# Optimization experiments

Hardware: AMD Instinct MI355X
Metric: run time of the kernel (lower is better)

The kernel has to match this reference:

```python
import jax, jax.numpy as jnp
import numpy as np
import math

B, L, C, H, CP = 2, 512, 576, 8, 128
C3 = C // 3            # 192
DK = C // H            # 72
DK3 = DK // 3          # 24
DIV = math.sqrt(DK)


def _ln(x, w, b, eps=1e-6):
    m = jnp.mean(x, axis=-1, keepdims=True)
    v = jnp.mean(jnp.square(x - m), axis=-1, keepdims=True)
    return (x - m) * jax.lax.rsqrt(v + eps) * w + b


def setup_inputs() -> dict:
    key = jax.random.key(0)
    ks = jax.random.split(key, 12)
    s = 0.05
    def n(k, shape):
        return jax.random.normal(k, shape, jnp.float32) * s
    return {
        "x": jax.random.normal(ks[0], (B, L, C), jnp.float32),
        "pairX": jax.random.normal(ks[1], (B, L, L, CP), jnp.float32),
        "g": jnp.ones((1,), jnp.float32),
        "ln1_w": jnp.ones((C,), jnp.float32), "ln1_b": jnp.zeros((C,), jnp.float32),
        "ln2_w": jnp.ones((CP,), jnp.float32), "ln2_b": jnp.zeros((CP,), jnp.float32),
        "Wq": n(ks[2], (C3, C3)), "bq": jnp.zeros((C3,), jnp.float32),
        "Wk": n(ks[3], (C3, C3)), "bk": jnp.zeros((C3,), jnp.float32),
        "Wv": n(ks[4], (C3, C3)), "bv": jnp.zeros((C3,), jnp.float32),
        "Wg": n(ks[5], (C3, C3)), "bg": jnp.zeros((C3,), jnp.float32),
        "conv_w": n(ks[6], (3, H, H, 5, 5)), "conv_b": jnp.zeros((3, H), jnp.float32),
        "Wp": n(ks[7], (CP, H)), "bp": jnp.zeros((H,), jnp.float32),
        "Wpr": n(ks[8], (H, CP)), "bpr": jnp.zeros((CP,), jnp.float32),
        "Wo": n(ks[9], (C, C)), "bo": jnp.zeros((C,), jnp.float32),
    }


def reference(x, pairX, g, ln1_w, ln1_b, ln2_w, ln2_b, Wq, bq, Wk, bk, Wv, bv,
              Wg, bg, conv_w, conv_b, Wp, bp, Wpr, bpr, Wo, bo):
    ori_x = x
    xn = _ln(x, ln1_w, ln1_b)                      # [B,L,C]
    pn = _ln(pairX, ln2_w, ln2_b)                  # [B,L,L,CP]

    # split channels into 3 groups: [B,3,L,C3]
    xs = xn.reshape(B, L, 3, C3).transpose(0, 2, 1, 3)

    def proj(W, b):
        y = xs @ W + b                              # [B,3,L,C3]
        return y.reshape(B, 3, L, H, DK3).transpose(0, 1, 3, 2, 4)  # [B,3,H,L,DK3]

    q = proj(Wq, bq)
    k = proj(Wk, bk)
    v = proj(Wv, bv)
    gate = proj(Wg, bg)

    qkMatrix = jnp.einsum('bchld,bchmd->bchlm', q, k)  # [B,3,H,L,L]
    pairBias = (pn @ Wp + bp).transpose(0, 3, 1, 2)[:, None]  # [B,1,H,L,L]
    oriQK = qkMatrix + pairBias                     # [B,3,H,L,L]

    # 3-channel 5x5 conv refinement, summed over the 3 branches -> [B,1,H,L,L]
    dn = ('NCHW', 'OIHW', 'NCHW')
    convQK = sum(
        jax.lax.conv_general_dilated(oriQK[:, i], conv_w[i], (1, 1), 'SAME',
                                     dimension_numbers=dn)
        + conv_b[i][None, :, None, None]
        for i in range(3)
    )[:, None]

    qk = (oriQK + convQK) / DIV                     # [B,3,H,L,L]
    score = jax.nn.softmax(qk, axis=-1)
    h_outs = jnp.einsum('bchlm,bchmd->bchld', score, v) * jax.nn.sigmoid(gate)
    h_outs = h_outs.transpose(0, 3, 1, 2, 4).reshape(B, L, C)

    rawScoreMean = jax.nn.gelu(jnp.mean(qk, axis=1).transpose(0, 2, 3, 1),
                               approximate=False)   # [B,L,L,H]
    out1 = (h_outs @ Wo + bo) + ori_x * g
    out2 = rawScoreMean @ Wpr + bpr                 # [B,L,L,CP]
    return out1, out2
```

## Files before the change

kernel.cpp:

```cpp
#include <hip/hip_runtime.h>
#include <hip/hip_bf16.h>

#define BDIM 2
#define LDIM 512
#define CDIM 576
#define HDIM 8
#define CPD  128
#define DK3  24
#define INV_DIV 0.117851130197757920f

static constexpr size_t OFF_Q    = 0;
static constexpr size_t OFF_K    = 589824;
static constexpr size_t OFF_V    = 1179648;
static constexpr size_t OFF_G    = 1769472;
static constexpr size_t OFF_BIAS = 2359296;
static constexpr size_t OFF_ORI  = OFF_BIAS + 4194304;
static constexpr size_t OFF_QK   = OFF_ORI + 12582912;
static constexpr size_t OFF_H    = OFF_QK + 12582912;
static constexpr size_t OFF_WPH  = OFF_H + 589824;
static constexpr size_t OFF_CS   = OFF_WPH + 1024;
static constexpr size_t OFF_XN   = OFF_QK;

__device__ __forceinline__ float gelu_exact(float v) {
    return 0.5f * v * (1.f + erff(v * 0.70710678118654752f));
}

__global__ __launch_bounds__(256) void k_prep(
    const float* __restrict__ ln2w, const float* __restrict__ ln2b,
    const float* __restrict__ Wp, const float* __restrict__ bp,
    float* __restrict__ wph, float* __restrict__ csum)
{
    __shared__ float wl[1024];
    const int tid = threadIdx.x;
    for (int i = tid; i < 1024; i += 256) {
        int h = i >> 7, d = i & 127;
        float v = ln2w[d] * Wp[d * 8 + h];
        wl[i] = v; wph[i] = v;
    }
    __syncthreads();
    const int h = tid >> 5, c4 = tid & 31;
    float p = wl[h * 128 + c4 * 4] + wl[h * 128 + c4 * 4 + 1]
            + wl[h * 128 + c4 * 4 + 2] + wl[h * 128 + c4 * 4 + 3];
#pragma unroll
    for (int o = 1; o < 32; o <<= 1) p += __shfl_xor(p, o);
    if (c4 == 0) csum[h] = p;
    float q = 0.f;
#pragma unroll
    for (int k = 0; k < 4; ++k) { int d = c4 * 4 + k; q = fmaf(ln2b[d], Wp[d * 8 + h], q); }
#pragma unroll
    for (int o = 1; o < 32; o <<= 1) q += __shfl_xor(q, o);
    if (c4 == 0) csum[8 + h] = q + bp[h];
}

__global__ __launch_bounds__(256) void k_ln(
    const float* __restrict__ x, const float* __restrict__ ln1w, const float* __restrict__ ln1b,
    float* __restrict__ xn)
{
    const int tid = threadIdx.x;
    const int wid = tid >> 6, lane = tid & 63;
    const int row = blockIdx.x * 4 + wid;
    const float* xr = x + (size_t)row * CDIM;
    float vals[9]; float s = 0.f, sq = 0.f;
#pragma unroll
    for (int u = 0; u < 9; ++u) {
        float v = xr[lane + 64 * u];
        vals[u] = v; s += v; sq += v * v;
    }
#pragma unroll
    for (int o = 32; o; o >>= 1) { s += __shfl_xor(s, o); sq += __shfl_xor(sq, o); }
    float m = s * (1.f / 576.f);
    float inv = rsqrtf(sq * (1.f / 576.f) - m * m + 1e-6f);
    float* xo = xn + (size_t)row * CDIM;
#pragma unroll
    for (int u = 0; u < 9; ++u) {
        int idx = lane + 64 * u;
        xo[idx] = (vals[u] - m) * inv * ln1w[idx] + ln1b[idx];
    }
}

__global__ __launch_bounds__(256) void k_proj(
    const float* __restrict__ xn,
    const float* __restrict__ Wq, const float* __restrict__ bq,
    const float* __restrict__ Wk, const float* __restrict__ bk,
    const float* __restrict__ Wv, const float* __restrict__ bv,
    const float* __restrict__ Wg, const float* __restrict__ bg,
    float* __restrict__ qo, float* __restrict__ ko, float* __restrict__ vo, float* __restrict__ go)
{
    __shared__ float As[192 * 64];
    __shared__ float Bs[32 * 192];
    const int tid = threadIdx.x;
    const int bx = blockIdx.x;
    const int mi = bx / 48, rem = bx % 48;
    const int g = rem >> 4, rb = rem & 15;
    const int row0 = rb * 64;

    const float* W  = mi == 0 ? Wq : mi == 1 ? Wk : mi == 2 ? Wv : Wg;
    const float* bb = mi == 0 ? bq : mi == 1 ? bk : mi == 2 ? bv : bg;
    float* op       = mi == 0 ? qo : mi == 1 ? ko : mi == 2 ? vo : go;

    {
        const int r = tid & 63, k4b = tid >> 6;
#pragma unroll
        for (int it = 0; it < 12; ++it) {
            int k4 = k4b + it * 4;
            float4 v = *(const float4*)&xn[(size_t)(row0 + r) * 576 + g * 192 + k4 * 4];
            As[(k4 * 4 + 0) * 64 + r] = v.x;
            As[(k4 * 4 + 1) * 64 + r] = v.y;
            As[(k4 * 4 + 2) * 64 + r] = v.z;
            As[(k4 * 4 + 3) * 64 + r] = v.w;
        }
    }

    const int rg = tid >> 4, cg = tid & 15;
    const int r0 = rg * 4, c0 = cg * 12;
    float acc[4][12] = {};

    for (int kk = 0; kk < 192; kk += 32) {
        __syncthreads();
#pragma unroll
        for (int i = 0; i < 6; ++i) {
            int f = tid + 256 * i;
            int k2 = f / 48, c4 = f % 48;
            *(float4*)&Bs[k2 * 192 + c4 * 4] = *(const float4*)&W[(size_t)(kk + k2) * 192 + c4 * 4];
        }
        __syncthreads();
#pragma unroll
        for (int k2 = 0; k2 < 32; ++k2) {
            const float4 a  = *(const float4*)&As[(kk + k2) * 64 + r0];
            const float4 b0 = *(const float4*)&Bs[k2 * 192 + c0];
            const float4 b1 = *(const float4*)&Bs[k2 * 192 + c0 + 4];
            const float4 b2 = *(const float4*)&Bs[k2 * 192 + c0 + 8];
            const float ar[4] = {a.x, a.y, a.z, a.w};
#pragma unroll
            for (int r = 0; r < 4; ++r) {
                acc[r][0] = fmaf(ar[r], b0.x, acc[r][0]);
                acc[r][1] = fmaf(ar[r], b0.y, acc[r][1]);
                acc[r][2] = fmaf(ar[r], b0.z, acc[r][2]);
                acc[r][3] = fmaf(ar[r], b0.w, acc[r][3]);
                acc[r][4] = fmaf(ar[r], b1.x, acc[r][4]);
                acc[r][5] = fmaf(ar[r], b1.y, acc[r][5]);
                acc[r][6] = fmaf(ar[r], b1.z, acc[r][6]);
                acc[r][7] = fmaf(ar[r], b1.w, acc[r][7]);
                acc[r][8] = fmaf(ar[r], b2.x, acc[r][8]);
                acc[r][9] = fmaf(ar[r], b2.y, acc[r][9]);
                acc[r][10] = fmaf(ar[r], b2.z, acc[r][10]);
                acc[r][11] = fmaf(ar[r], b2.w, acc[r][11]);
            }
        }
    }

    const int h = cg >> 1, d24 = (cg & 1) * 12;
    const float4 bj0 = *(const float4*)&bb[c0];
    const float4 bj1 = *(const float4*)&bb[c0 + 4];
    const float4 bj2 = *(const float4*)&bb[c0 + 8];
#pragma unroll
    for (int r = 0; r < 4; ++r) {
        int row = row0 + r0 + r;
        int b = row >> 9, l = row & 511;
        float* o = op + ((((size_t)b * 3 + g) * HDIM + h) * LDIM + l) * DK3 + d24;
        *(float4*)(o + 0) = make_float4(acc[r][0] + bj0.x, acc[r][1] + bj0.y,
                                        acc[r][2] + bj0.z, acc[r][3] + bj0.w);
        *(float4*)(o + 4) = make_float4(acc[r][4] + bj1.x, acc[r][5] + bj1.y,
                                        acc[r][6] + bj1.z, acc[r][7] + bj1.w);
        *(float4*)(o + 8) = make_float4(acc[r][8] + bj2.x, acc[r][9] + bj2.y,
                                        acc[r][10] + bj2.z, acc[r][11] + bj2.w);
    }
}

__global__ __launch_bounds__(256) void k_pairbias(
    const float* __restrict__ pairX, const float* __restrict__ wph,
    const float* __restrict__ csum, float* __restrict__ bias)
{
    const int row = blockIdx.x * 256 + threadIdx.x;
    const float* rp = pairX + (size_t)row * CPD;

    float acc[8] = {};
    float sum = 0.f, sumsq = 0.f;
    for (int s = 0; s < 8; ++s) {
        float rr[16];
        *(float4*)&rr[0]  = *(const float4*)(rp + s * 16 + 0);
        *(float4*)&rr[4]  = *(const float4*)(rp + s * 16 + 4);
        *(float4*)&rr[8]  = *(const float4*)(rp + s * 16 + 8);
        *(float4*)&rr[12] = *(const float4*)(rp + s * 16 + 12);
#pragma unroll
        for (int k = 0; k < 16; ++k) { sum += rr[k]; sumsq = fmaf(rr[k], rr[k], sumsq); }
        const float* wp_s = wph + s * 16;
#pragma unroll
        for (int h = 0; h < 8; ++h) {
            const float* w = wp_s + h * 128;
#pragma unroll
            for (int k = 0; k < 16; ++k) acc[h] = fmaf(rr[k], w[k], acc[h]);
        }
    }
    const float m = sum * (1.f / 128.f);
    const float inv = rsqrtf(sumsq * (1.f / 128.f) - m * m + 1e-6f);
    const int b = row >> 18;
    const int ij = row & 262143;
    float* bo = bias + ((size_t)b << 21) + ij;
#pragma unroll
    for (int h = 0; h < 8; ++h) {
        float o = inv * (acc[h] - m * csum[h]) + csum[8 + h];
        bo[(size_t)h << 18] = o;
    }
}

__global__ __launch_bounds__(256) void k_qkmat(
    const float* __restrict__ q, const float* __restrict__ k,
    const float* __restrict__ bias, float* __restrict__ oriQK)
{
    __shared__ float Kl[512 * 28];
    __shared__ float Ql[32 * 28];
    const int tid = threadIdx.x;
    const int bch = blockIdx.x >> 4;
    const int itile = blockIdx.x & 15;
    const float* kp = k + (size_t)bch * 512 * 24;
    const float* qp = q + (size_t)bch * 512 * 24 + (size_t)itile * 32 * 24;
    for (int idx = tid; idx < 512 * 24; idx += 256) {
        int j = idx / 24, d = idx - j * 24;
        Kl[j * 28 + d] = kp[idx];
    }
    for (int idx = tid; idx < 32 * 24; idx += 256) {
        int i = idx / 24, d = idx - i * 24;
        Ql[i * 28 + d] = qp[idx];
    }
    __syncthreads();

    const int ti = tid >> 4, tj = tid & 15;
    const int b = bch / 24, h = bch & 7;
    const float* biasp = bias + ((size_t)(b * 8 + h) * 512 + itile * 32) * 512;
    float* outp = oriQK + (size_t)bch * 262144 + (size_t)itile * 32 * 512;

    for (int cc = 0; cc < 4; ++cc) {
        float acc[2][8] = {};
#pragma unroll
        for (int d4 = 0; d4 < 6; ++d4) {
            const float4 q0 = *(const float4*)&Ql[(ti * 2 + 0) * 28 + d4 * 4];
            const float4 q1 = *(const float4*)&Ql[(ti * 2 + 1) * 28 + d4 * 4];
#pragma unroll
            for (int u = 0; u < 8; ++u) {
                const float4 kv = *(const float4*)&Kl[(cc * 128 + u * 16 + tj) * 28 + d4 * 4];
                acc[0][u] = fmaf(q0.x, kv.x, fmaf(q0.y, kv.y, fmaf(q0.z, kv.z, fmaf(q0.w, kv.w, acc[0][u]))));
                acc[1][u] = fmaf(q1.x, kv.x, fmaf(q1.y, kv.y, fmaf(q1.z, kv.z, fmaf(q1.w, kv.w, acc[1][u]))));
            }
        }
#pragma unroll
        for (int r = 0; r < 2; ++r) {
            int i = ti * 2 + r;
#pragma unroll
            for (int u = 0; u < 8; ++u) {
                int j = cc * 128 + u * 16 + tj;
                outp[(size_t)i * 512 + j] = acc[r][u] + biasp[(size_t)i * 512 + j];
            }
        }
    }
}

__global__ __launch_bounds__(256, 3) void k_conv(
    const float* __restrict__ oriQK, const float* __restrict__ convW, const float* __restrict__ convB,
    const float* __restrict__ Wpr, const float* __restrict__ bpr,
    float* __restrict__ qk, float* __restrict__ out2)
{
    __shared__ float smem[8 * 36 * 40];
    float* tile = smem;
    const int tid = threadIdx.x;
    const int bx = blockIdx.x;
    const int b = bx >> 8, rem = bx & 255;
    const int i0 = (rem >> 4) * 32, j0 = (rem & 15) * 32;

    const int jg = tid & 7, ii = tid >> 3;
    const int j4 = jg * 4;
    float acc[8][4] = {};
    float cen[3][8][4];

    for (int c = 0; c < 3; ++c) {
        __syncthreads();
        for (int idx = tid; idx < 8 * 1296; idx += 256) {
            int ch = idx / 1296;
            int r = idx - ch * 1296;
            int iw = r / 36, jw = r - iw * 36;
            int gi = i0 - 2 + iw, gj = j0 - 2 + jw;
            float v = 0.f;
            if ((unsigned)gi < 512u && (unsigned)gj < 512u)
                v = oriQK[((size_t)(b * 24 + c * 8 + ch) << 18) + ((size_t)gi << 9) + gj];
            tile[ch * 1440 + iw * 40 + jw] = v;
        }
        __syncthreads();

        const float* wb = convW + c * 1600;
        for (int hi = 0; hi < 8; ++hi) {
            const float* tch = &tile[hi * 1440];
#pragma unroll
            for (int kh = 0; kh < 5; ++kh) {
                const float* trow = &tch[(ii + kh) * 40 + j4];
                float v[8];
                *(float4*)&v[0] = *(const float4*)&trow[0];
                *(float4*)&v[4] = *(const float4*)&trow[4];
                if (kh == 2) {
                    cen[c][hi][0] = v[2]; cen[c][hi][1] = v[3];
                    cen[c][hi][2] = v[4]; cen[c][hi][3] = v[5];
                }
#pragma unroll
                for (int kw = 0; kw < 5; ++kw) {
                    const float* wt = wb + hi * 25 + kh * 5 + kw;
                    const float w0 = wt[0],    w1 = wt[200],  w2 = wt[400],  w3 = wt[600];
                    const float w4 = wt[800],  w5 = wt[1000], w6 = wt[1200], w7 = wt[1400];
#pragma unroll
                    for (int j = 0; j < 4; ++j) {
                        float vv = v[kw + j];
                        acc[0][j] = fmaf(w0, vv, acc[0][j]);
                        acc[1][j] = fmaf(w1, vv, acc[1][j]);
                        acc[2][j] = fmaf(w2, vv, acc[2][j]);
                        acc[3][j] = fmaf(w3, vv, acc[3][j]);
                        acc[4][j] = fmaf(w4, vv, acc[4][j]);
                        acc[5][j] = fmaf(w5, vv, acc[5][j]);
                        acc[6][j] = fmaf(w6, vv, acc[6][j]);
                        acc[7][j] = fmaf(w7, vv, acc[7][j]);
                    }
                }
            }
        }
    }
    __syncthreads();

    float* gql = smem;
    const int gi = i0 + ii, gj = j0 + j4;
    float* qkb = qk + ((size_t)(b * 24) << 18) + ((size_t)gi << 9) + gj;
#pragma unroll
    for (int h = 0; h < 8; ++h) {
        float cv = convB[h] + convB[8 + h] + convB[16 + h];
        float cj[4];
#pragma unroll
        for (int j = 0; j < 4; ++j) cj[j] = acc[h][j] + cv;
        float mm[4] = {};
#pragma unroll
        for (int c = 0; c < 3; ++c) {
            float4 o = make_float4((cen[c][h][0] + cj[0]) * INV_DIV,
                                   (cen[c][h][1] + cj[1]) * INV_DIV,
                                   (cen[c][h][2] + cj[2]) * INV_DIV,
                                   (cen[c][h][3] + cj[3]) * INV_DIV);
            *(float4*)(qkb + ((size_t)(c * 8 + h) << 18)) = o;
#pragma unroll
            for (int j = 0; j < 4; ++j) mm[j] += cen[c][h][j];
        }
        float4 gv4;
        gv4.x = gelu_exact((mm[0] * (1.f / 3.f) + cj[0]) * INV_DIV);
        gv4.y = gelu_exact((mm[1] * (1.f / 3.f) + cj[1]) * INV_DIV);
        gv4.z = gelu_exact((mm[2] * (1.f / 3.f) + cj[2]) * INV_DIV);
        gv4.w = gelu_exact((mm[3] * (1.f / 3.f) + cj[3]) * INV_DIV);
        *(float4*)&gql[h * 1024 + ii * 32 + j4] = gv4;
    }
    __syncthreads();

    const int pq = tid & 31, pg = tid >> 5;
    float4 wv[8];
#pragma unroll
    for (int h = 0; h < 8; ++h) wv[h] = *(const float4*)&Wpr[h * 128 + pq * 4];
    const float4 bv = *(const float4*)&bpr[pq * 4];

    for (int it = 0; it < 128; ++it) {
        int pos = it * 8 + pg;
        float g8[8];
#pragma unroll
        for (int h = 0; h < 8; ++h) g8[h] = gql[h * 1024 + pos];
        float4 o = bv;
        o.x += g8[0]*wv[0].x + g8[1]*wv[1].x + g8[2]*wv[2].x + g8[3]*wv[3].x
             + g8[4]*wv[4].x + g8[5]*wv[5].x + g8[6]*wv[6].x + g8[7]*wv[7].x;
        o.y += g8[0]*wv[0].y + g8[1]*wv[1].y + g8[2]*wv[2].y + g8[3]*wv[3].y
             + g8[4]*wv[4].y + g8[5]*wv[5].y + g8[6]*wv[6].y + g8[7]*wv[7].y;
        o.z += g8[0]*wv[0].z + g8[1]*wv[1].z + g8[2]*wv[2].z + g8[3]*wv[3].z
             + g8[4]*wv[4].z + g8[5]*wv[5].z + g8[6]*wv[6].z + g8[7]*wv[7].z;
        o.w += g8[0]*wv[0].w + g8[1]*wv[1].w + g8[2]*wv[2].w + g8[3]*wv[3].w
             + g8[4]*wv[4].w + g8[5]*wv[5].w + g8[6]*wv[6].w + g8[7]*wv[7].w;
        int oi = i0 + (pos >> 5), oj = j0 + (pos & 31);
        *(float4*)&out2[(((size_t)(b * 512 + oi) << 9) + oj) * 128 + pq * 4] = o;
    }
}

__global__ __launch_bounds__(256) void k_softmax_pv(
    const float* __restrict__ qk, const float* __restrict__ v, const float* __restrict__ gate,
    float* __restrict__ houts)
{
    __shared__ float Vl[512 * 28];
    const int tid = threadIdx.x;
    const int bch = blockIdx.x >> 4, itile = blockIdx.x & 15;
    const float* vp = v + (size_t)bch * (512 * 24);
    for (int idx = tid; idx < 512 * 24; idx += 256) {
        int j = idx / 24, d = idx - j * 24;
        Vl[j * 28 + d] = vp[idx];
    }
    __syncthreads();

    const int wid = tid >> 6, lane = tid & 63;
    const int b = bch / 24, c = (bch % 24) >> 3, h = bch & 7;
    const int tg = lane >> 3;
    for (int rr = 0; rr < 8; ++rr) {
        const int i = itile * 32 + wid * 8 + rr;
        const float* row = qk + ((size_t)bch * 512 + i) * 512;
        float e[8]; float mx = -1e30f;
#pragma unroll
        for (int u = 0; u < 8; ++u) { e[u] = row[lane + 64 * u]; mx = fmaxf(mx, e[u]); }
#pragma unroll
        for (int o = 32; o; o >>= 1) mx = fmaxf(mx, __shfl_xor(mx, o));
        float s = 0.f;
#pragma unroll
        for (int u = 0; u < 8; ++u) { e[u] = __expf(e[u] - mx); s += e[u]; }
#pragma unroll
        for (int o = 32; o; o >>= 1) s += __shfl_xor(s, o);
        float inv = 1.f / s;

        float4 a4[6] = {};
#pragma unroll
        for (int u = 0; u < 8; ++u) {
            float p = e[u] * inv;
            const float* vr = &Vl[(u * 64 + lane) * 28];
#pragma unroll
            for (int k = 0; k < 6; ++k) {
                float4 vv = *(const float4*)(vr + 4 * k);
                a4[k].x = fmaf(p, vv.x, a4[k].x);
                a4[k].y = fmaf(p, vv.y, a4[k].y);
                a4[k].z = fmaf(p, vv.z, a4[k].z);
                a4[k].w = fmaf(p, vv.w, a4[k].w);
            }
        }
#pragma unroll
        for (int k = 0; k < 6; ++k) {
            a4[k].x += __shfl_xor(a4[k].x, 8);  a4[k].y += __shfl_xor(a4[k].y, 8);
            a4[k].z += __shfl_xor(a4[k].z, 8);  a4[k].w += __shfl_xor(a4[k].w, 8);
            a4[k].x += __shfl_xor(a4[k].x, 16); a4[k].y += __shfl_xor(a4[k].y, 16);
            a4[k].z += __shfl_xor(a4[k].z, 16); a4[k].w += __shfl_xor(a4[k].w, 16);
            a4[k].x += __shfl_xor(a4[k].x, 32); a4[k].y += __shfl_xor(a4[k].y, 32);
            a4[k].z += __shfl_xor(a4[k].z, 32); a4[k].w += __shfl_xor(a4[k].w, 32);
        }
        const float af[24] = {
            a4[0].x, a4[0].y, a4[0].z, a4[0].w, a4[1].x, a4[1].y, a4[1].z, a4[1].w,
            a4[2].x, a4[2].y, a4[2].z, a4[2].w, a4[3].x, a4[3].y, a4[3].z, a4[3].w,
            a4[4].x, a4[4].y, a4[4].z, a4[4].w, a4[5].x, a4[5].y, a4[5].z, a4[5].w };
        float w0 = tg==0?af[0]:tg==1?af[3]:tg==2?af[6]:tg==3?af[9]:tg==4?af[12]:tg==5?af[15]:tg==6?af[18]:af[21];
        float w1 = tg==0?af[1]:tg==1?af[4]:tg==2?af[7]:tg==3?af[10]:tg==4?af[13]:tg==5?af[16]:tg==6?af[19]:af[22];
        float w2 = tg==0?af[2]:tg==1?af[5]:tg==2?af[8]:tg==3?af[11]:tg==4?af[14]:tg==5?af[17]:tg==6?af[20]:af[23];
#pragma unroll
        for (int o = 1; o < 8; o <<= 1) {
            w0 += __shfl_xor(w0, o);
            w1 += __shfl_xor(w1, o);
            w2 += __shfl_xor(w2, o);
        }
        if ((lane & 7) == 0) {
            const int d0 = tg * 3;
            const float* gp = gate + ((size_t)bch * 512 + i) * 24 + d0;
            float* op = houts + ((size_t)(b * 512 + i)) * 576 + c * 192 + h * 24 + d0;
            op[0] = w0 / (1.f + __expf(-gp[0]));
            op[1] = w1 / (1.f + __expf(-gp[1]));
            op[2] = w2 / (1.f + __expf(-gp[2]));
        }
    }
}

__global__ __launch_bounds__(256) void k_out1(
    const float* __restrict__ houts, const float* __restrict__ Wo, const float* __restrict__ bo,
    const float* __restrict__ x, const float* __restrict__ gsc,
    float* __restrict__ out1)
{
    __shared__ float As[32 * 33];
    __shared__ float Bs[32 * 64];
    const int tid = threadIdx.x;
    const int mt = blockIdx.x / 9, nt = blockIdx.x % 9;
    const int m0 = mt * 32, n0 = nt * 64;
    const int tn = tid & 15, tm = tid >> 4;
    float acc[2][4] = {};

    for (int kk = 0; kk < 576; kk += 32) {
        {
            int idx = tid;
#pragma unroll
            for (int i = 0; i < 4; ++i, idx += 256) {
                int k2 = idx & 31, m = idx >> 5;
                As[m * 33 + k2] = houts[(size_t)(m0 + m) * 576 + kk + k2];
            }
        }
        {
            int idx = tid;
#pragma unroll
            for (int i = 0; i < 8; ++i, idx += 256) {
                int n = idx & 63, k2 = idx >> 6;
                Bs[k2 * 64 + n] = Wo[(size_t)(kk + k2) * 576 + n0 + n];
            }
        }
        __syncthreads();
#pragma unroll
        for (int k2 = 0; k2 < 32; ++k2) {
            float a0 = As[(tm * 2 + 0) * 33 + k2];
            float a1 = As[(tm * 2 + 1) * 33 + k2];
            const float4 bv = *(const float4*)&Bs[k2 * 64 + tn * 4];
            acc[0][0] += a0 * bv.x; acc[0][1] += a0 * bv.y; acc[0][2] += a0 * bv.z; acc[0][3] += a0 * bv.w;
            acc[1][0] += a1 * bv.x; acc[1][1] += a1 * bv.y; acc[1][2] += a1 * bv.z; acc[1][3] += a1 * bv.w;
        }
        __syncthreads();
    }

    const float gv = gsc[0];
    const float4 b4 = *(const float4*)&bo[n0 + tn * 4];
#pragma unroll
    for (int r = 0; r < 2; ++r) {
        size_t row = (size_t)m0 + tm * 2 + r;
        size_t off = row * 576 + n0 + tn * 4;
        const float4 x4 = *(const float4*)&x[off];
        float4 o;
        o.x = acc[r][0] + b4.x + x4.x * gv;
        o.y = acc[r][1] + b4.y + x4.y * gv;
        o.z = acc[r][2] + b4.z + x4.z * gv;
        o.w = acc[r][3] + b4.w + x4.w * gv;
        *(float4*)&out1[off] = o;
    }
}

extern "C" void kernel_launch(void* const* d_in, const int* in_sizes, int n_in,
                              void* d_out, int out_size, void* d_ws, size_t ws_size,
                              hipStream_t stream) {
    const float* x     = (const float*)d_in[0];
    const float* pairX = (const float*)d_in[1];
    const float* g     = (const float*)d_in[2];
    const float* ln1w  = (const float*)d_in[3];
    const float* ln1b  = (const float*)d_in[4];
    const float* ln2w  = (const float*)d_in[5];
    const float* ln2b  = (const float*)d_in[6];
    const float* Wq    = (const float*)d_in[7];
    const float* bq    = (const float*)d_in[8];
    const float* Wk    = (const float*)d_in[9];
    const float* bk    = (const float*)d_in[10];
    const float* Wv    = (const float*)d_in[11];
    const float* bv    = (const float*)d_in[12];
    const float* Wg    = (const float*)d_in[13];
    const float* bg    = (const float*)d_in[14];
    const float* convW = (const float*)d_in[15];
    const float* convB = (const float*)d_in[16];
    const float* Wp    = (const float*)d_in[17];
    const float* bp    = (const float*)d_in[18];
    const float* Wpr   = (const float*)d_in[19];
    const float* bpr   = (const float*)d_in[20];
    const float* Wo    = (const float*)d_in[21];
    const float* bo    = (const float*)d_in[22];

    float* ws   = (float*)d_ws;
    float* q    = ws + OFF_Q;
    float* k    = ws + OFF_K;
    float* vv   = ws + OFF_V;
    float* gt   = ws + OFF_G;
    float* bias = ws + OFF_BIAS;
    float* ori  = ws + OFF_ORI;
    float* qkb  = ws + OFF_QK;
    float* xn   = ws + OFF_XN;
    float* hout = ws + OFF_H;
    float* wph  = ws + OFF_WPH;
    float* csum = ws + OFF_CS;

    float* out1 = (float*)d_out;
    float* out2 = out1 + 589824;

    k_prep<<<dim3(1), dim3(256), 0, stream>>>(ln2w, ln2b, Wp, bp, wph, csum);
    k_ln<<<dim3(256), dim3(256), 0, stream>>>(x, ln1w, ln1b, xn);
    k_proj<<<dim3(192), dim3(256), 0, stream>>>(xn, Wq, bq, Wk, bk, Wv, bv, Wg, bg,
                                                q, k, vv, gt);
    k_pairbias<<<dim3(2048), dim3(256), 0, stream>>>(pairX, wph, csum, bias);
    k_qkmat<<<dim3(768), dim3(256), 0, stream>>>(q, k, bias, ori);
    k_conv<<<dim3(512), dim3(256), 0, stream>>>(ori, convW, convB, Wpr, bpr, qkb, out2);
    k_softmax_pv<<<dim3(768), dim3(256), 0, stream>>>(qkb, vv, gt, hout);
    k_out1<<<dim3(288), dim3(256), 0, stream>>>(hout, Wo, bo, x, g, out1);
}
```

Measured before the change: 492.2 us.

## Shrink conv tile to 16x16 with one pixel per thread and single-pass staging

The 5x5 conv kernel now uses 16x16 output tiles instead of 32x32, with one output pixel per thread instead of four. It stages all 24 channels of the halo tile into shared memory once rather than in three per-branch passes, and the grid grows from 512 to 2048 blocks. The aim is more parallelism and fewer block-level syncs, and center values are re-read from shared memory instead of being held in registers. In exchange, halo overhead rises (20x20 loaded per 16x16 output) and register-level reuse of weights across neighbouring pixels is lost, so each weight load now feeds one FMA instead of four.

```diff
diff --git a/kernel.cpp b/kernel.cpp
--- a/kernel.cpp
+++ b/kernel.cpp
@@ -260,95 +260,66 @@
     const float* __restrict__ Wpr, const float* __restrict__ bpr,
     float* __restrict__ qk, float* __restrict__ out2)
 {
-    __shared__ float smem[8 * 36 * 40];
-    float* tile = smem;
+    __shared__ float smem[24 * 20 * 24];
     const int tid = threadIdx.x;
     const int bx = blockIdx.x;
-    const int b = bx >> 8, rem = bx & 255;
-    const int i0 = (rem >> 4) * 32, j0 = (rem & 15) * 32;
-
-    const int jg = tid & 7, ii = tid >> 3;
-    const int j4 = jg * 4;
-    float acc[8][4] = {};
-    float cen[3][8][4];
-
+    const int b = bx >> 10, rem = bx & 1023;
+    const int i0 = (rem >> 5) * 16, j0 = (rem & 31) * 16;
+
+    for (int idx = tid; idx < 9600; idx += 256) {
+        int ch = idx / 400;
+        int r = idx - ch * 400;
+        int iw = r / 20, jw = r - iw * 20;
+        int gi = i0 - 2 + iw, gj = j0 - 2 + jw;
+        float v = 0.f;
+        if ((unsigned)gi < 512u && (unsigned)gj < 512u)
+            v = oriQK[((size_t)(b * 24 + ch) << 18) + ((size_t)gi << 9) + gj];
+        smem[ch * 480 + iw * 24 + jw] = v;
+    }
+    __syncthreads();
+
+    const int ii = tid >> 4, jc = tid & 15;
+    float acc[8] = {};
     for (int c = 0; c < 3; ++c) {
-        __syncthreads();
-        for (int idx = tid; idx < 8 * 1296; idx += 256) {
-            int ch = idx / 1296;
-            int r = idx - ch * 1296;
-            int iw = r / 36, jw = r - iw * 36;
-            int gi = i0 - 2 + iw, gj = j0 - 2 + jw;
-            float v = 0.f;
-            if ((unsigned)gi < 512u && (unsigned)gj < 512u)
-                v = oriQK[((size_t)(b * 24 + c * 8 + ch) << 18) + ((size_t)gi << 9) + gj];
-            tile[ch * 1440 + iw * 40 + jw] = v;
-        }
-        __syncthreads();
-
-        const float* wb = convW + c * 1600;
         for (int hi = 0; hi < 8; ++hi) {
-            const float* tch = &tile[hi * 1440];
+            const float* tch = &smem[(c * 8 + hi) * 480];
+            const float* wb = convW + c * 1600 + hi * 25;
 #pragma unroll
             for (int kh = 0; kh < 5; ++kh) {
-                const float* trow = &tch[(ii + kh) * 40 + j4];
-                float v[8];
-                *(float4*)&v[0] = *(const float4*)&trow[0];
-                *(float4*)&v[4] = *(const float4*)&trow[4];
-                if (kh == 2) {
-                    cen[c][hi][0] = v[2]; cen[c][hi][1] = v[3];
-                    cen[c][hi][2] = v[4]; cen[c][hi][3] = v[5];
+                const float* trow = &tch[(ii + kh) * 24 + jc];
+                const float v0 = trow[0], v1 = trow[1], v2 = trow[2], v3 = trow[3], v4 = trow[4];
+#pragma unroll
+                for (int kw = 0; kw < 5; ++kw) {
+                    const float vv = kw == 0 ? v0 : kw == 1 ? v1 : kw == 2 ? v2 : kw == 3 ? v3 : v4;
+                    const float* wt = wb + kh * 5 + kw;
+#pragma unroll
+                    for (int h = 0; h < 8; ++h)
+                        acc[h] = fmaf(wt[h * 200], vv, acc[h]);
                 }
-#pragma unroll
-                for (int kw = 0; kw < 5; ++kw) {
-                    const float* wt = wb + hi * 25 + kh * 5 + kw;
-                    const float w0 = wt[0],    w1 = wt[200],  w2 = wt[400],  w3 = wt[600];
-                    const float w4 = wt[800],  w5 = wt[1000], w6 = wt[1200], w7 = wt[1400];
-#pragma unroll
-                    for (int j = 0; j < 4; ++j) {
-                        float vv = v[kw + j];
-                        acc[0][j] = fmaf(w0, vv, acc[0][j]);
-                        acc[1][j] = fmaf(w1, vv, acc[1][j]);
-                        acc[2][j] = fmaf(w2, vv, acc[2][j]);
-                        acc[3][j] = fmaf(w3, vv, acc[3][j]);
-                        acc[4][j] = fmaf(w4, vv, acc[4][j]);
-                        acc[5][j] = fmaf(w5, vv, acc[5][j]);
-                        acc[6][j] = fmaf(w6, vv, acc[6][j]);
-                        acc[7][j] = fmaf(w7, vv, acc[7][j]);
-                    }
-                }
-            }
-        }
+            }
+        }
+    }
+
+    const int gi = i0 + ii, gj = j0 + jc;
+    float* qkb = qk + ((size_t)(b * 24) << 18) + ((size_t)gi << 9) + gj;
+    float gv[8];
+#pragma unroll
+    for (int h = 0; h < 8; ++h) {
+        const float cj = acc[h] + convB[h] + convB[8 + h] + convB[16 + h];
+        float mm = 0.f;
+#pragma unroll
+        for (int c = 0; c < 3; ++c) {
+            float cenv = smem[(c * 8 + h) * 480 + (ii + 2) * 24 + jc + 2];
+            qkb[(size_t)(c * 8 + h) << 18] = (cenv + cj) * INV_DIV;
+            mm += cenv;
+        }
+        gv[h] = gelu_exact((mm * (1.f / 3.f) + cj) * INV_DIV);
     }
     __syncthreads();
 
     float* gql = smem;
-    const int gi = i0 + ii, gj = j0 + j4;
-    float* qkb = qk + ((size_t)(b * 24) << 18) + ((size_t)gi << 9) + gj;
-#pragma unroll
-    for (int h = 0; h < 8; ++h) {
-        float cv = convB[h] + convB[8 + h] + convB[16 + h];
-        float cj[4];
-#pragma unroll
-        for (int j = 0; j < 4; ++j) cj[j] = acc[h][j] + cv;
-        float mm[4] = {};
-#pragma unroll
-        for (int c = 0; c < 3; ++c) {
-            float4 o = make_float4((cen[c][h][0] + cj[0]) * INV_DIV,
-                                   (cen[c][h][1] + cj[1]) * INV_DIV,
-                                   (cen[c][h][2] + cj[2]) * INV_DIV,
-                                   (cen[c][h][3] + cj[3]) * INV_DIV);
-            *(float4*)(qkb + ((size_t)(c * 8 + h) << 18)) = o;
-#pragma unroll
-            for (int j = 0; j < 4; ++j) mm[j] += cen[c][h][j];
-        }
-        float4 gv4;
-        gv4.x = gelu_exact((mm[0] * (1.f / 3.f) + cj[0]) * INV_DIV);
-        gv4.y = gelu_exact((mm[1] * (1.f / 3.f) + cj[1]) * INV_DIV);
-        gv4.z = gelu_exact((mm[2] * (1.f / 3.f) + cj[2]) * INV_DIV);
-        gv4.w = gelu_exact((mm[3] * (1.f / 3.f) + cj[3]) * INV_DIV);
-        *(float4*)&gql[h * 1024 + ii * 32 + j4] = gv4;
-    }
+#pragma unroll
+    for (int h = 0; h < 8; ++h) gql[h * 256 + tid] = gv[h];
     __syncthreads();
 
     const int pq = tid & 31, pg = tid >> 5;
@@ -357,11 +328,11 @@
     for (int h = 0; h < 8; ++h) wv[h] = *(const float4*)&Wpr[h * 128 + pq * 4];
     const float4 bv = *(const float4*)&bpr[pq * 4];
 
-    for (int it = 0; it < 128; ++it) {
+    for (int it = 0; it < 32; ++it) {
         int pos = it * 8 + pg;
         float g8[8];
 #pragma unroll
-        for (int h = 0; h < 8; ++h) g8[h] = gql[h * 1024 + pos];
+        for (int h = 0; h < 8; ++h) g8[h] = gql[h * 256 + pos];
         float4 o = bv;
         o.x += g8[0]*wv[0].x + g8[1]*wv[1].x + g8[2]*wv[2].x + g8[3]*wv[3].x
              + g8[4]*wv[4].x + g8[5]*wv[5].x + g8[6]*wv[6].x + g8[7]*wv[7].x;
@@ -371,7 +342,7 @@
              + g8[4]*wv[4].z + g8[5]*wv[5].z + g8[6]*wv[6].z + g8[7]*wv[7].z;
         o.w += g8[0]*wv[0].w + g8[1]*wv[1].w + g8[2]*wv[2].w + g8[3]*wv[3].w
              + g8[4]*wv[4].w + g8[5]*wv[5].w + g8[6]*wv[6].w + g8[7]*wv[7].w;
-        int oi = i0 + (pos >> 5), oj = j0 + (pos & 31);
+        int oi = i0 + (pos >> 4), oj = j0 + (pos & 15);
         *(float4*)&out2[(((size_t)(b * 512 + oi) << 9) + oj) * 128 + pq * 4] = o;
     }
 }
@@ -562,7 +533,7 @@
                                                 q, k, vv, gt);
     k_pairbias<<<dim3(2048), dim3(256), 0, stream>>>(pairX, wph, csum, bias);
     k_qkmat<<<dim3(768), dim3(256), 0, stream>>>(q, k, bias, ori);
-    k_conv<<<dim3(512), dim3(256), 0, stream>>>(ori, convW, convB, Wpr, bpr, qkb, out2);
+    k_conv<<<dim3(2048), dim3(256), 0, stream>>>(ori, convW, convB, Wpr, bpr, qkb, out2);
     k_softmax_pv<<<dim3(768), dim3(256), 0, stream>>>(qkb, vv, gt, hout);
     k_out1<<<dim3(288), dim3(256), 0, stream>>>(hout, Wo, bo, x, g, out1);
 }
```

Measured after the change: 542.6 us. 10.2% more time.
